# Kernel optimization log

Hardware: AMD Instinct MI355X
Metric: run time of the kernel (lower is better)

The kernel has to match this reference:

```python
import jax, jax.numpy as jnp
import numpy as np

N = 100000   # nodes
E = 1600000  # edges (before self-loops)
F_IN = 128
H = 64
G = 512      # graphs in batch


def _add_self_loops(edge_index, n):
    loop = jnp.arange(n, dtype=edge_index.dtype)
    src = jnp.concatenate([edge_index[0], loop])
    dst = jnp.concatenate([edge_index[1], loop])
    return src, dst


def _gcn_norm(src, dst, n):
    # PyG GCNConv: deg over targets with self-loops, norm = d^-1/2[src]*d^-1/2[dst]
    deg = jax.ops.segment_sum(jnp.ones_like(dst, dtype=jnp.float32), dst, num_segments=n)
    dinv = jnp.where(deg > 0, jax.lax.rsqrt(deg), 0.0)
    return dinv[src] * dinv[dst]


def _gcn_conv(x, src, dst, norm, W, b):
    xw = x @ W                                # [N, H]
    msg = xw[src] * norm[:, None]             # [E+N, H] gather + scale
    out = jax.ops.segment_sum(msg, dst, num_segments=x.shape[0])
    return out + b


def setup_inputs() -> dict:
    key = jax.random.key(0)
    ks = jax.random.split(key, 9)
    x = jax.random.normal(ks[0], (N, F_IN), dtype=jnp.float32)
    edge_index = jax.random.randint(ks[1], (2, E), 0, N, dtype=jnp.int32)
    batch = jnp.sort(jax.random.randint(ks[2], (N,), 0, G, dtype=jnp.int32))
    s1 = 1.0 / np.sqrt(F_IN)
    s2 = 1.0 / np.sqrt(H)
    W1 = jax.random.uniform(ks[3], (F_IN, H), jnp.float32, -s1, s1)
    b1 = jnp.zeros((H,), jnp.float32)
    W2 = jax.random.uniform(ks[4], (H, H), jnp.float32, -s2, s2)
    b2 = jnp.zeros((H,), jnp.float32)
    Wl = jax.random.uniform(ks[5], (H, 1), jnp.float32, -s2, s2)
    bl = jnp.zeros((1,), jnp.float32)
    return {"x": x, "edge_index": edge_index, "batch": batch,
            "W1": W1, "b1": b1, "W2": W2, "b2": b2, "Wl": Wl, "bl": bl}


def reference(x, edge_index, batch, W1, b1, W2, b2, Wl, bl):
    n = x.shape[0]
    src, dst = _add_self_loops(edge_index, n)
    norm = _gcn_norm(src, dst, n)
    h = jax.nn.relu(_gcn_conv(x, src, dst, norm, W1, b1))
    h = jax.nn.relu(_gcn_conv(h, src, dst, norm, W2, b2))
    # global mean pool over graphs
    sums = jax.ops.segment_sum(h, batch, num_segments=G)          # [G, H]
    cnt = jax.ops.segment_sum(jnp.ones((n,), jnp.float32), batch, num_segments=G)
    pooled = sums / jnp.maximum(cnt, 1.0)[:, None]
    return jax.nn.sigmoid(pooled @ Wl + bl)                        # [G, 1]
```

## Files before the change

kernel.cpp:

```cpp
#include <hip/hip_runtime.h>
#include <hip/hip_bf16.h>
#include <cmath>

#define F_IN 128
#define HDIM 64
#define NPB 128
#define NB1 512
#define CAP 2560

typedef __attribute__((ext_vector_type(8))) short bf16x8;
typedef __attribute__((ext_vector_type(4))) float f32x4;
typedef __attribute__((ext_vector_type(2))) float f32x2;

__device__ __forceinline__ float bf2f(unsigned short u) {
    union { unsigned int i; float f; } v; v.i = ((unsigned int)u) << 16; return v.f;
}
__device__ __forceinline__ unsigned short f2bf(float f) {
    __hip_bfloat16 h = __float2bfloat16(f);
    union { __hip_bfloat16 h; unsigned short u; } c; c.h = h; return c.u;
}
__device__ __forceinline__ unsigned char f2fp8(float f) {
    int p = __builtin_amdgcn_cvt_pk_fp8_f32(f, f, 0, false);
    return (unsigned char)(p & 0xff);
}
__device__ __forceinline__ void fp8x8_acc(uint2 v, float* a) {
    f32x2 f;
    f = __builtin_amdgcn_cvt_pk_f32_fp8(v.x, false); a[0] += f.x; a[1] += f.y;
    f = __builtin_amdgcn_cvt_pk_f32_fp8(v.x, true);  a[2] += f.x; a[3] += f.y;
    f = __builtin_amdgcn_cvt_pk_f32_fp8(v.y, false); a[4] += f.x; a[5] += f.y;
    f = __builtin_amdgcn_cvt_pk_f32_fp8(v.y, true);  a[6] += f.x; a[7] += f.y;
}
__device__ __forceinline__ void fp8x8_acc_m(uint2 v, float m, float* a) {
    f32x2 f;
    f = __builtin_amdgcn_cvt_pk_f32_fp8(v.x, false); a[0] = fmaf(f.x, m, a[0]); a[1] = fmaf(f.y, m, a[1]);
    f = __builtin_amdgcn_cvt_pk_f32_fp8(v.x, true);  a[2] = fmaf(f.x, m, a[2]); a[3] = fmaf(f.y, m, a[3]);
    f = __builtin_amdgcn_cvt_pk_f32_fp8(v.y, false); a[4] = fmaf(f.x, m, a[4]); a[5] = fmaf(f.y, m, a[5]);
    f = __builtin_amdgcn_cvt_pk_f32_fp8(v.y, true);  a[6] = fmaf(f.x, m, a[6]); a[7] = fmaf(f.y, m, a[7]);
}

__device__ __forceinline__ void gather_rows(const int* __restrict__ col,
                                            const uint2* __restrict__ xws,
                                            int L, int s, int end, float* a) {
    int e = s;
    for (; e + 8 <= end; e += 8) {
        uint2 v0 = xws[(size_t)col[e + 0] * 8 + L];
        uint2 v1 = xws[(size_t)col[e + 1] * 8 + L];
        uint2 v2 = xws[(size_t)col[e + 2] * 8 + L];
        uint2 v3 = xws[(size_t)col[e + 3] * 8 + L];
        uint2 v4 = xws[(size_t)col[e + 4] * 8 + L];
        uint2 v5 = xws[(size_t)col[e + 5] * 8 + L];
        uint2 v6 = xws[(size_t)col[e + 6] * 8 + L];
        uint2 v7 = xws[(size_t)col[e + 7] * 8 + L];
        fp8x8_acc(v0, a); fp8x8_acc(v1, a); fp8x8_acc(v2, a); fp8x8_acc(v3, a);
        fp8x8_acc(v4, a); fp8x8_acc(v5, a); fp8x8_acc(v6, a); fp8x8_acc(v7, a);
    }
    if (e < end) {
        int last = end - 1;
        uint2 v0 = xws[(size_t)col[e]               * 8 + L];
        uint2 v1 = xws[(size_t)col[min(e + 1, last)] * 8 + L];
        uint2 v2 = xws[(size_t)col[min(e + 2, last)] * 8 + L];
        uint2 v3 = xws[(size_t)col[min(e + 3, last)] * 8 + L];
        uint2 v4 = xws[(size_t)col[min(e + 4, last)] * 8 + L];
        uint2 v5 = xws[(size_t)col[min(e + 5, last)] * 8 + L];
        uint2 v6 = xws[(size_t)col[min(e + 6, last)] * 8 + L];
        uint2 v7 = xws[(size_t)col[min(e + 7, last)] * 8 + L];
        fp8x8_acc(v0, a);
        fp8x8_acc_m(v1, (e + 1 < end) ? 1.0f : 0.0f, a);
        fp8x8_acc_m(v2, (e + 2 < end) ? 1.0f : 0.0f, a);
        fp8x8_acc_m(v3, (e + 3 < end) ? 1.0f : 0.0f, a);
        fp8x8_acc_m(v4, (e + 4 < end) ? 1.0f : 0.0f, a);
        fp8x8_acc_m(v5, (e + 5 < end) ? 1.0f : 0.0f, a);
        fp8x8_acc_m(v6, (e + 6 < end) ? 1.0f : 0.0f, a);
        fp8x8_acc_m(v7, (e + 7 < end) ? 1.0f : 0.0f, a);
    }
}


__launch_bounds__(256)
__global__ void k_init(const float* __restrict__ W1, const float* __restrict__ W2,
                       unsigned short* __restrict__ w1t, unsigned short* __restrict__ w2t,
                       const int* __restrict__ batch, int* __restrict__ gstart,
                       int n, int G, int* __restrict__ gcnt) {
    int t = blockIdx.x * 256 + threadIdx.x;
    if (t < F_IN * 64) {
        int c = t & 63, k = t >> 6;
        w1t[c * F_IN + k] = f2bf(W1[t]);
        return;
    }
    t -= F_IN * 64;
    if (t < HDIM * 64) {
        int c = t & 63, k = t >> 6;
        w2t[c * HDIM + k] = f2bf(W2[t]);
        return;
    }
    t -= HDIM * 64;
    if (t <= G) {
        int g = t;
        int lo = 0, hi = n;
        while (lo < hi) {
            int mid = (lo + hi) >> 1;
            if (batch[mid] < g) lo = mid + 1; else hi = mid;
        }
        gstart[g] = lo;
        return;
    }
    t -= G + 1;
    if (t < 1024) gcnt[t] = 0;
}


__launch_bounds__(256)
__global__ void p_place(const int* __restrict__ src, const int* __restrict__ dst,
                        int* __restrict__ gcnt, int* __restrict__ pairs,
                        int E, int nbuk, int chunk) {
    __shared__ int hist[1024];
    __shared__ int cur[1024];
    int tid = threadIdx.x;
    for (int i = tid; i < nbuk; i += 256) hist[i] = 0;
    __syncthreads();
    int lo = blockIdx.x * chunk, hi = min(E, lo + chunk);
    for (int e = lo + tid; e < hi; e += 256)
        atomicAdd(&hist[dst[e] >> 7], 1);
    __syncthreads();
    for (int i = tid; i < nbuk; i += 256) {
        int c = hist[i];
        cur[i] = i * CAP + (c ? atomicAdd(&gcnt[i], c) : 0);
    }
    __syncthreads();
    for (int e = lo + tid; e < hi; e += 256) {
        int d = dst[e];
        int pos = atomicAdd(&cur[d >> 7], 1);
        pairs[pos] = (src[e] << 7) | (d & 127);
    }
}


__launch_bounds__(256)
__global__ void p2_csr(const int* __restrict__ pairs, const int* __restrict__ bucket_cnt,
                       float* __restrict__ dinv, int* __restrict__ col,
                       int4* __restrict__ slot_hdr, int n) {
    __shared__ int plds[CAP];
    __shared__ int dl[128];
    __shared__ int sc[128];
    __shared__ int cur[128];
    __shared__ int h64[64];
    __shared__ int s64[64];
    int b = blockIdx.x, tid = threadIdx.x;
    int nlo = b << 7;
    int eb = b * CAP;
    int cnt = bucket_cnt[b];
    if (tid < 128) dl[tid] = 0;
    if (tid < 64) h64[tid] = 0;
    __syncthreads();
    for (int i = tid; i < cnt; i += 256) {
        int v = pairs[eb + i];
        plds[i] = v;
        atomicAdd(&dl[v & 127], 1);
    }
    __syncthreads();
    int d0 = 0, excl = 0;
    if (tid < 128) { d0 = dl[tid]; sc[tid] = d0; }
    __syncthreads();
    for (int off = 1; off < 128; off <<= 1) {
        int a = (tid >= off && tid < 128) ? sc[tid - off] : 0;
        __syncthreads();
        if (tid < 128) sc[tid] += a;
        __syncthreads();
    }
    if (tid < 128) {
        excl = sc[tid] - d0;
        int node = nlo + tid;
        if (node < n) dinv[node] = rsqrtf((float)(d0 + 1));
        cur[tid] = eb + excl;
        atomicAdd(&h64[min(d0, 63)], 1);
    }
    __syncthreads();
    if (tid == 0) { int run = 0; for (int i = 0; i < 64; ++i) { s64[i] = run; run += h64[i]; } }
    __syncthreads();
    if (tid < 64) h64[tid] = 0;
    __syncthreads();
    if (tid < 128) {
        int node = nlo + tid;
        int bin = min(d0, 63);
        int pos = s64[bin] + atomicAdd(&h64[bin], 1);
        int4 hdr;
        hdr.x = (node < n) ? node : 0x7fffffff;
        hdr.y = eb + excl;
        hdr.z = d0;
        hdr.w = __float_as_int(rsqrtf((float)(d0 + 1)));
        slot_hdr[nlo + pos] = hdr;
    }
    __syncthreads();
    for (int i = tid; i < cnt; i += 256) {
        unsigned int v = (unsigned int)plds[i];
        int pos = atomicAdd(&cur[v & 127], 1);
        col[pos] = (int)(v >> 7);
    }
}


template <int K>
__launch_bounds__(256)
__global__ void matmul_mfma(const float* __restrict__ X, const unsigned short* __restrict__ Wt,
                            const float* __restrict__ dinv, unsigned char* __restrict__ out,
                            int n) {
    constexpr int KS  = K / 32;
    constexpr int LDX = K + 8;
    __shared__ unsigned short Xs[64 * LDX];
    __shared__ unsigned short Ws[64 * LDX];
    int tid = threadIdx.x;
    int rowbase = blockIdx.x * 64;
    for (int i = tid; i < 64 * (K / 8); i += 256) {
        int r = i / (K / 8), ch = i % (K / 8);
        *(bf16x8*)(Ws + r * LDX + ch * 8) = ((const bf16x8*)Wt)[i];
    }
    {
        const float4* X4 = (const float4*)X;
        for (int i = tid; i < 64 * (K / 4); i += 256) {
            int r = i / (K / 4), k4 = i % (K / 4);
            ushort4 u = { 0, 0, 0, 0 };
            int gr = rowbase + r;
            if (gr < n) {
                float4 v = X4[(size_t)gr * (K / 4) + k4];
                u.x = f2bf(v.x); u.y = f2bf(v.y); u.z = f2bf(v.z); u.w = f2bf(v.w);
            }
            *(ushort4*)(Xs + r * LDX + k4 * 4) = u;
        }
    }
    __syncthreads();
    int wave = tid >> 6, lane = tid & 63;
    int q = lane >> 4, nn = lane & 15;
    f32x4 acc[4] = {{0,0,0,0},{0,0,0,0},{0,0,0,0},{0,0,0,0}};
    int mrow = wave * 16 + nn;
#pragma unroll
    for (int s = 0; s < KS; ++s) {
        bf16x8 af = *(const bf16x8*)(Xs + mrow * LDX + s * 32 + q * 8);
#pragma unroll
        for (int c = 0; c < 4; ++c) {
            bf16x8 bf = *(const bf16x8*)(Ws + (c * 16 + nn) * LDX + s * 32 + q * 8);
            acc[c] = __builtin_amdgcn_mfma_f32_16x16x32_bf16(af, bf, acc[c], 0, 0, 0);
        }
    }
#pragma unroll
    for (int r = 0; r < 4; ++r) {
        int row = rowbase + wave * 16 + q * 4 + r;
        if (row >= n) continue;
        float dv = dinv[row];
#pragma unroll
        for (int c = 0; c < 4; ++c)
            out[(size_t)row * HDIM + c * 16 + nn] = f2fp8(acc[c][r] * dv);
    }
}


__launch_bounds__(256)
__global__ void gather1_mm2(const int4* __restrict__ slot_hdr, const int* __restrict__ col,
                            const uint2* __restrict__ xws, const float* __restrict__ bias,
                            const unsigned short* __restrict__ w2t,
                            unsigned char* __restrict__ out8, int nslots, int n) {
    __shared__ unsigned short Hs[32 * 72];
    __shared__ unsigned short Ws[64 * 72];
    __shared__ int   snode[32];
    __shared__ float sdinv[32];

    int tid = threadIdx.x;
    int ls = tid >> 3;
    int L  = tid & 7;
    int slot = blockIdx.x * 32 + ls;

    for (int i = tid; i < 64 * 8; i += 256) {
        int r = i >> 3, ch = i & 7;
        *(bf16x8*)(Ws + r * 72 + ch * 8) = ((const bf16x8*)w2t)[i];
    }

    int node = 0x7fffffff;
    float dv = 0.0f;
    float a[8] = {0, 0, 0, 0, 0, 0, 0, 0};
    if (slot < nslots) {
        int4 hdr = slot_hdr[slot];
        node = hdr.x;
        if (node < n) {
            dv = __int_as_float(hdr.w);
            fp8x8_acc(xws[(size_t)node * 8 + L], a);
            gather_rows(col, xws, L, hdr.y, hdr.y + hdr.z, a);
        }
    }
    if (L == 0) { snode[ls] = node; sdinv[ls] = dv; }
    {
        int f0 = L * 8;
        bf16x8 o;
        if (node < n) {
#pragma unroll
            for (int j = 0; j < 8; ++j)
                o[j] = (short)f2bf(fmaxf(fmaf(a[j], dv, bias[f0 + j]), 0.0f));
        } else {
            short z[8] = {0,0,0,0,0,0,0,0};
            o = *(bf16x8*)z;
        }
        *(bf16x8*)(Hs + ls * 72 + L * 8) = o;
    }
    __syncthreads();

    int wave = tid >> 6, lane = tid & 63;
    int q = lane >> 4, nn = lane & 15;
    int mt  = wave & 1;
    int nt0 = (wave >> 1) * 2;
    f32x4 acc[2] = {{0,0,0,0},{0,0,0,0}};
#pragma unroll
    for (int s = 0; s < 2; ++s) {
        bf16x8 af = *(const bf16x8*)(Hs + (mt * 16 + nn) * 72 + s * 32 + q * 8);
#pragma unroll
        for (int t = 0; t < 2; ++t) {
            bf16x8 bf = *(const bf16x8*)(Ws + ((nt0 + t) * 16 + nn) * 72 + s * 32 + q * 8);
            acc[t] = __builtin_amdgcn_mfma_f32_16x16x32_bf16(af, bf, acc[t], 0, 0, 0);
        }
    }
#pragma unroll
    for (int r = 0; r < 4; ++r) {
        int lslot = mt * 16 + q * 4 + r;
        int nd = snode[lslot];
        if (nd >= n) continue;
        float dvr = sdinv[lslot];
#pragma unroll
        for (int t = 0; t < 2; ++t)
            out8[(size_t)nd * HDIM + (nt0 + t) * 16 + nn] = f2fp8(acc[t][r] * dvr);
    }
}


__launch_bounds__(256)
__global__ void csr_gather8_fp8(const int4* __restrict__ slot_hdr, const int* __restrict__ col,
                                const uint2* __restrict__ xws, const float* __restrict__ bias,
                                bf16x8* __restrict__ outb, int nslots, int n) {
    int t = blockIdx.x * 256 + threadIdx.x;
    int slot = t >> 3;
    if (slot >= nslots) return;
    int L = t & 7;
    int4 hdr = slot_hdr[slot];
    int node = hdr.x;
    if (node >= n) return;
    float dv = __int_as_float(hdr.w);

    float a[8] = {0, 0, 0, 0, 0, 0, 0, 0};
    fp8x8_acc(xws[(size_t)node * 8 + L], a);
    gather_rows(col, xws, L, hdr.y, hdr.y + hdr.z, a);

    int f0 = L * 8;
    bf16x8 o;
#pragma unroll
    for (int j = 0; j < 8; ++j)
        o[j] = (short)f2bf(fmaxf(fmaf(a[j], dv, bias[f0 + j]), 0.0f));
    outb[(size_t)node * 8 + L] = o;
}


__launch_bounds__(256)
__global__ void pool_head(const unsigned short* __restrict__ h, const int* __restrict__ gstart,
                          const float* __restrict__ Wl, const float* __restrict__ bl,
                          float* __restrict__ out, int G) {
    int g = blockIdx.x;
    int s = gstart[g], e = gstart[g + 1];
    int f  = threadIdx.x & 63;
    int rg = threadIdx.x >> 6;
    float acc = 0.0f;
    for (int i = s + rg; i < e; i += 4)
        acc += bf2f(h[(size_t)i * HDIM + f]);
    __shared__ float red[4][HDIM];
    red[rg][f] = acc;
    __syncthreads();
    if (rg == 0) {
        float v = (red[0][f] + red[1][f]) + (red[2][f] + red[3][f]);
        float c = fmaxf((float)(e - s), 1.0f);
        v = v * Wl[f] * (1.0f / c);
#pragma unroll
        for (int off = 32; off; off >>= 1) v += __shfl_down(v, off, 64);
        if (f == 0) out[g] = 1.0f / (1.0f + expf(-(v + bl[0])));
    }
}


extern "C" void kernel_launch(void* const* d_in, const int* in_sizes, int n_in,
                              void* d_out, int out_size, void* d_ws, size_t ws_size,
                              hipStream_t stream) {
    const float* x   = (const float*)d_in[0];
    const int* ei    = (const int*)d_in[1];
    const int* batch = (const int*)d_in[2];
    const float* W1  = (const float*)d_in[3];
    const float* b1  = (const float*)d_in[4];
    const float* W2  = (const float*)d_in[5];
    const float* b2  = (const float*)d_in[6];
    const float* Wl  = (const float*)d_in[7];
    const float* bl  = (const float*)d_in[8];
    float* out = (float*)d_out;

    const int n = in_sizes[0] / F_IN;
    const int E = in_sizes[1] / 2;
    const int G = out_size;

    const int* srcp = ei;
    const int* dstp = ei + E;

    int nbuk = (n + NPB - 1) / NPB;
    int nslots = nbuk * NPB;

    char* wsb = (char*)d_ws;
    auto alloc = [&](size_t bytes) { char* p = wsb; wsb += (bytes + 255) & ~(size_t)255; return p; };
    float* dinv       = (float*)alloc((size_t)n * 4);
    int4*  slot_hdr   = (int4*)alloc((size_t)nslots * 16);
    int*   gcnt       = (int*)alloc(1024 * 4);
    int*   pairs      = (int*)alloc((size_t)nbuk * CAP * 4);
    int*   colx       = (int*)alloc((size_t)nbuk * CAP * 4);
    unsigned short* w1t  = (unsigned short*)alloc((size_t)F_IN * HDIM * 2);
    unsigned short* w2t  = (unsigned short*)alloc((size_t)HDIM * HDIM * 2);
    unsigned char*  xws8 = (unsigned char*)alloc((size_t)n * HDIM);
    unsigned char*  xws8b= (unsigned char*)alloc((size_t)n * HDIM);
    unsigned short* xh2  = (unsigned short*)alloc((size_t)n * HDIM * 2);
    int*   gstart     = (int*)alloc(((size_t)G + 1) * 4);

    const int TB = 256;
    int gMM  = (n + 63) / 64;
    int chunk = (E + NB1 - 1) / NB1;
    int gG8  = (nslots * 8 + TB - 1) / TB;
    int gS   = (nslots + 31) / 32;
    int initWork = F_IN * 64 + HDIM * 64 + (G + 1) + 1024;
    int gInit = (initWork + TB - 1) / TB;

    k_init<<<gInit, TB, 0, stream>>>(W1, W2, w1t, w2t, batch, gstart, n, G, gcnt);
    p_place<<<NB1, TB, 0, stream>>>(srcp, dstp, gcnt, pairs, E, nbuk, chunk);
    p2_csr<<<nbuk, TB, 0, stream>>>(pairs, gcnt, dinv, colx, slot_hdr, n);
    matmul_mfma<F_IN><<<gMM, TB, 0, stream>>>(x, w1t, dinv, xws8, n);
    gather1_mm2<<<gS, TB, 0, stream>>>(slot_hdr, colx, (const uint2*)xws8,
                                       b1, w2t, xws8b, nslots, n);
    csr_gather8_fp8<<<gG8, TB, 0, stream>>>(slot_hdr, colx, (const uint2*)xws8b,
                                            b2, (bf16x8*)xh2, nslots, n);
    pool_head<<<G, TB, 0, stream>>>(xh2, gstart, Wl, bl, out, G);
}
```

Before: 233.0 us.

## Build CSR via global per-node degree atomics instead of bucketed two-pass sort

Result: slower. 393.6 us (+68.9%).

```diff
diff --git a/kernel.cpp b/kernel.cpp
--- a/kernel.cpp
+++ b/kernel.cpp
@@ -5,7 +5,6 @@
 #define F_IN 128
 #define HDIM 64
 #define NPB 128
-#define NB1 512
 #define CAP 2560
 
 typedef __attribute__((ext_vector_type(8))) short bf16x8;
@@ -80,7 +79,7 @@
 __global__ void k_init(const float* __restrict__ W1, const float* __restrict__ W2,
                        unsigned short* __restrict__ w1t, unsigned short* __restrict__ w2t,
                        const int* __restrict__ batch, int* __restrict__ gstart,
-                       int n, int G, int* __restrict__ gcnt) {
+                       int n, int G, int* __restrict__ deg) {
     int t = blockIdx.x * 256 + threadIdx.x;
     if (t < F_IN * 64) {
         int c = t & 63, k = t >> 6;
@@ -105,96 +104,85 @@
         return;
     }
     t -= G + 1;
-    if (t < 1024) gcnt[t] = 0;
-}
-
-
-__launch_bounds__(256)
-__global__ void p_place(const int* __restrict__ src, const int* __restrict__ dst,
-                        int* __restrict__ gcnt, int* __restrict__ pairs,
-                        int E, int nbuk, int chunk) {
-    __shared__ int hist[1024];
-    __shared__ int cur[1024];
-    int tid = threadIdx.x;
-    for (int i = tid; i < nbuk; i += 256) hist[i] = 0;
-    __syncthreads();
-    int lo = blockIdx.x * chunk, hi = min(E, lo + chunk);
-    for (int e = lo + tid; e < hi; e += 256)
-        atomicAdd(&hist[dst[e] >> 7], 1);
-    __syncthreads();
-    for (int i = tid; i < nbuk; i += 256) {
-        int c = hist[i];
-        cur[i] = i * CAP + (c ? atomicAdd(&gcnt[i], c) : 0);
-    }
-    __syncthreads();
-    for (int e = lo + tid; e < hi; e += 256) {
-        int d = dst[e];
-        int pos = atomicAdd(&cur[d >> 7], 1);
-        pairs[pos] = (src[e] << 7) | (d & 127);
-    }
-}
-
-
-__launch_bounds__(256)
-__global__ void p2_csr(const int* __restrict__ pairs, const int* __restrict__ bucket_cnt,
-                       float* __restrict__ dinv, int* __restrict__ col,
-                       int4* __restrict__ slot_hdr, int n) {
-    __shared__ int plds[CAP];
-    __shared__ int dl[128];
+    if (t < n) deg[t] = 0;
+}
+
+
+__launch_bounds__(256)
+__global__ void k_deg(const int* __restrict__ dst, int* __restrict__ deg, int E) {
+    int e = (blockIdx.x * 256 + threadIdx.x) * 4;
+    if (e + 4 <= E) {
+        int4 d = *(const int4*)(dst + e);
+        atomicAdd(&deg[d.x], 1);
+        atomicAdd(&deg[d.y], 1);
+        atomicAdd(&deg[d.z], 1);
+        atomicAdd(&deg[d.w], 1);
+    } else {
+        for (; e < E; ++e) atomicAdd(&deg[dst[e]], 1);
+    }
+}
+
+
+__launch_bounds__(128)
+__global__ void p2_hdr(const int* __restrict__ deg, float* __restrict__ dinv,
+                       int* __restrict__ curpos, int4* __restrict__ slot_hdr, int n) {
     __shared__ int sc[128];
-    __shared__ int cur[128];
     __shared__ int h64[64];
     __shared__ int s64[64];
     int b = blockIdx.x, tid = threadIdx.x;
     int nlo = b << 7;
     int eb = b * CAP;
-    int cnt = bucket_cnt[b];
-    if (tid < 128) dl[tid] = 0;
+    int node = nlo + tid;
+    int d0 = (node < n) ? deg[node] : 0;
+    sc[tid] = d0;
     if (tid < 64) h64[tid] = 0;
     __syncthreads();
-    for (int i = tid; i < cnt; i += 256) {
-        int v = pairs[eb + i];
-        plds[i] = v;
-        atomicAdd(&dl[v & 127], 1);
-    }
-    __syncthreads();
-    int d0 = 0, excl = 0;
-    if (tid < 128) { d0 = dl[tid]; sc[tid] = d0; }
-    __syncthreads();
     for (int off = 1; off < 128; off <<= 1) {
-        int a = (tid >= off && tid < 128) ? sc[tid - off] : 0;
+        int a = (tid >= off) ? sc[tid - off] : 0;
         __syncthreads();
-        if (tid < 128) sc[tid] += a;
+        sc[tid] += a;
         __syncthreads();
     }
-    if (tid < 128) {
-        excl = sc[tid] - d0;
-        int node = nlo + tid;
-        if (node < n) dinv[node] = rsqrtf((float)(d0 + 1));
-        cur[tid] = eb + excl;
-        atomicAdd(&h64[min(d0, 63)], 1);
-    }
+    int excl = sc[tid] - d0;
+    float dv = rsqrtf((float)(d0 + 1));
+    if (node < n) {
+        dinv[node] = dv;
+        curpos[node] = eb + excl;
+    }
+    atomicAdd(&h64[min(d0, 63)], 1);
     __syncthreads();
     if (tid == 0) { int run = 0; for (int i = 0; i < 64; ++i) { s64[i] = run; run += h64[i]; } }
     __syncthreads();
     if (tid < 64) h64[tid] = 0;
     __syncthreads();
-    if (tid < 128) {
-        int node = nlo + tid;
-        int bin = min(d0, 63);
-        int pos = s64[bin] + atomicAdd(&h64[bin], 1);
-        int4 hdr;
-        hdr.x = (node < n) ? node : 0x7fffffff;
-        hdr.y = eb + excl;
-        hdr.z = d0;
-        hdr.w = __float_as_int(rsqrtf((float)(d0 + 1)));
-        slot_hdr[nlo + pos] = hdr;
-    }
-    __syncthreads();
-    for (int i = tid; i < cnt; i += 256) {
-        unsigned int v = (unsigned int)plds[i];
-        int pos = atomicAdd(&cur[v & 127], 1);
-        col[pos] = (int)(v >> 7);
+    int bin = min(d0, 63);
+    int pos = s64[bin] + atomicAdd(&h64[bin], 1);
+    int4 hdr;
+    hdr.x = (node < n) ? node : 0x7fffffff;
+    hdr.y = eb + excl;
+    hdr.z = d0;
+    hdr.w = __float_as_int(dv);
+    slot_hdr[nlo + pos] = hdr;
+}
+
+
+__launch_bounds__(256)
+__global__ void k_place(const int* __restrict__ src, const int* __restrict__ dst,
+                        int* __restrict__ curpos, int* __restrict__ col, int E) {
+    int e = (blockIdx.x * 256 + threadIdx.x) * 4;
+    if (e + 4 <= E) {
+        int4 d = *(const int4*)(dst + e);
+        int4 s = *(const int4*)(src + e);
+        int p0 = atomicAdd(&curpos[d.x], 1);
+        int p1 = atomicAdd(&curpos[d.y], 1);
+        int p2 = atomicAdd(&curpos[d.z], 1);
+        int p3 = atomicAdd(&curpos[d.w], 1);
+        col[p0] = s.x; col[p1] = s.y; col[p2] = s.z; col[p3] = s.w;
+    } else {
+        for (; e < E; ++e) {
+            int p = atomicAdd(&curpos[dst[e]], 1);
+            col[p] = src[e];
+        }
     }
 }
 
@@ -407,8 +395,8 @@
     auto alloc = [&](size_t bytes) { char* p = wsb; wsb += (bytes + 255) & ~(size_t)255; return p; };
     float* dinv       = (float*)alloc((size_t)n * 4);
     int4*  slot_hdr   = (int4*)alloc((size_t)nslots * 16);
-    int*   gcnt       = (int*)alloc(1024 * 4);
-    int*   pairs      = (int*)alloc((size_t)nbuk * CAP * 4);
+    int*   deg        = (int*)alloc((size_t)n * 4);
+    int*   curpos     = (int*)alloc((size_t)n * 4);
     int*   colx       = (int*)alloc((size_t)nbuk * CAP * 4);
     unsigned short* w1t  = (unsigned short*)alloc((size_t)F_IN * HDIM * 2);
     unsigned short* w2t  = (unsigned short*)alloc((size_t)HDIM * HDIM * 2);
@@ -419,15 +407,16 @@
 
     const int TB = 256;
     int gMM  = (n + 63) / 64;
-    int chunk = (E + NB1 - 1) / NB1;
+    int gE4  = (E / 4 + TB - 1) / TB;
     int gG8  = (nslots * 8 + TB - 1) / TB;
     int gS   = (nslots + 31) / 32;
-    int initWork = F_IN * 64 + HDIM * 64 + (G + 1) + 1024;
+    int initWork = F_IN * 64 + HDIM * 64 + (G + 1) + n;
     int gInit = (initWork + TB - 1) / TB;
 
-    k_init<<<gInit, TB, 0, stream>>>(W1, W2, w1t, w2t, batch, gstart, n, G, gcnt);
-    p_place<<<NB1, TB, 0, stream>>>(srcp, dstp, gcnt, pairs, E, nbuk, chunk);
-    p2_csr<<<nbuk, TB, 0, stream>>>(pairs, gcnt, dinv, colx, slot_hdr, n);
+    k_init<<<gInit, TB, 0, stream>>>(W1, W2, w1t, w2t, batch, gstart, n, G, deg);
+    k_deg<<<gE4, TB, 0, stream>>>(dstp, deg, E);
+    p2_hdr<<<nbuk, 128, 0, stream>>>(deg, dinv, curpos, slot_hdr, n);
+    k_place<<<gE4, TB, 0, stream>>>(srcp, dstp, curpos, colx, E);
     matmul_mfma<F_IN><<<gMM, TB, 0, stream>>>(x, w1t, dinv, xws8, n);
     gather1_mm2<<<gS, TB, 0, stream>>>(slot_hdr, colx, (const uint2*)xws8,
                                        b1, w2t, xws8b, nslots, n);
```
